# Kernel tuning notes

Measured on AMD Instinct MI355X. Metric: run time of the kernel, lower is better.

The kernel has to match this reference:

```python
import jax, jax.numpy as jnp
import numpy as np

EMBED_DIM = 2048
NUM_HEADS = 16
HEAD_DIM = EMBED_DIM // NUM_HEADS
BATCH, SEQ = 4, 4096


def setup_inputs() -> dict:
    key = jax.random.key(0)
    k1, k2, k3, k4 = jax.random.split(key, 4)
    scale = 1.0 / np.sqrt(EMBED_DIM)
    x = jax.random.normal(k1, (BATCH, SEQ, EMBED_DIM), dtype=jnp.float32)
    W_qkv = jax.random.normal(k2, (EMBED_DIM, 3 * EMBED_DIM), dtype=jnp.float32) * scale
    W_out = jax.random.normal(k3, (EMBED_DIM, EMBED_DIM), dtype=jnp.float32) * scale
    b_out = jax.random.normal(k4, (EMBED_DIM,), dtype=jnp.float32) * 0.01
    return {"x": x, "W_qkv": W_qkv, "W_out": W_out, "b_out": b_out}


def reference(x, W_qkv, W_out, b_out):
    b, s, _ = x.shape
    # qkv: (b, s, 3, h, d)
    qkv = (x @ W_qkv).reshape(b, s, 3, NUM_HEADS, HEAD_DIM)
    q, k, v = qkv[:, :, 0], qkv[:, :, 1], qkv[:, :, 2]
    # NOTE: faithful to source — scores mix HEADS per token: (b, s, h, h)
    scores = jnp.einsum('bshd,bsHd->bshH', q, k) / jnp.sqrt(jnp.float32(HEAD_DIM))
    w = jax.nn.softmax(scores, axis=-1)
    attn = jnp.einsum('bshH,bsHd->bshd', w, v).reshape(b, s, EMBED_DIM)
    return attn @ W_out + b_out
```

## Files before the change

### kernel.cpp

```cpp
#include <hip/hip_runtime.h>
#include <hip/hip_bf16.h>
#include <cstdint>


#define TOKENS 16384
#define EMB    2048
#define NQKV   6144

typedef __bf16 bf16x8_t __attribute__((ext_vector_type(8)));
typedef float  f32x4_t  __attribute__((ext_vector_type(4)));

#define GLOAD16(gsrc, ldst)                                                    \
  __builtin_amdgcn_global_load_lds(                                            \
      (const __attribute__((address_space(1))) void*)(uintptr_t)(gsrc),        \
      (__attribute__((address_space(3))) void*)(uint32_t)(uintptr_t)(ldst),    \
      16, 0, 0)

static __device__ __forceinline__ unsigned short f32_to_bf16_bits(float f) {
  union { float f; uint32_t u; } x; x.f = f;
  uint32_t u = x.u;
  u += 0x7fffu + ((u >> 16) & 1u);
  return (unsigned short)(u >> 16);
}

__global__ __launch_bounds__(256) void prep(
    const float4* __restrict__ x4, ushort4* __restrict__ xb4,
    const float* __restrict__ Wqkv, unsigned short* __restrict__ wqkvT,
    const float* __restrict__ Wout, unsigned short* __restrict__ woutT) {
  const int b = blockIdx.x;
  const int t = threadIdx.x;
  if (b < 2048) {
    const int n4 = 33554432 / 4;
    const int stride = 2048 * 256;
    for (int i = b * 256 + t; i < n4; i += stride) {
      float4 v = x4[i];
      ushort4 o;
      o.x = f32_to_bf16_bits(v.x);
      o.y = f32_to_bf16_bits(v.y);
      o.z = f32_to_bf16_bits(v.z);
      o.w = f32_to_bf16_bits(v.w);
      xb4[i] = o;
    }
    return;
  }
  __shared__ float tile[32][33];
  const float* in;
  unsigned short* out;
  int R, C, bxt, byt;
  if (b < 14336) {
    const int bb = b - 2048;
    in = Wqkv; out = wqkvT; R = 2048; C = 6144;
    bxt = bb % 192; byt = bb / 192;
  } else {
    const int bb = b - 14336;
    in = Wout; out = woutT; R = 2048; C = 2048;
    bxt = bb % 64; byt = bb / 64;
  }
  const int bx = bxt * 32;
  const int by = byt * 32;
  const int tx = t & 31;
  const int ty = t >> 5;
#pragma unroll
  for (int j = 0; j < 32; j += 8)
    tile[ty + j][tx] = in[(size_t)(by + ty + j) * C + bx + tx];
  __syncthreads();
#pragma unroll
  for (int j = 0; j < 32; j += 8)
    out[(size_t)(bx + ty + j) * R + by + tx] = f32_to_bf16_bits(tile[tx][ty + j]);
}

template <bool OUT_BF16>
__global__ __launch_bounds__(512, 1) void gemm_bt(
    const unsigned short* __restrict__ A,
    const unsigned short* __restrict__ BT,
    unsigned short* __restrict__ Cb,
    float* __restrict__ Cf,
    const float* __restrict__ bias,
    int M, int N) {
  constexpr int K = 2048;
  constexpr int BK = 64;
  constexpr int NKT = K / BK;
  __shared__ __align__(16) char lds[131072];

  const int nbx = N / 256;
  const int nwg = gridDim.x;
  const int bid = blockIdx.x;
  const int swzb = (bid & 7) * (nwg >> 3) + (bid >> 3);
  const int by = swzb / nbx;
  const int bx = swzb % nbx;

  const int t    = threadIdx.x;
  const int lane = t & 63;
  const int wid  = t >> 6;
  const int wr   = wid >> 2;
  const int wc   = wid & 3;
  const int lr   = lane & 15;
  const int g    = lane >> 4;

  const unsigned short* aSrc = A  + (size_t)by * 256 * K;
  const unsigned short* bSrc = BT + (size_t)bx * 256 * K;

  int aoff[2], boff[2];
#pragma unroll
  for (int i = 0; i < 2; ++i) {
    const int p   = (i * 512 + t) * 16;
    const int lo  = p ^ (((p >> 7) & 7) << 4);
    const int rih = lo >> 7;
    const int kbe = (lo & 127) >> 1;
    aoff[i] = (((rih >> 6) << 7) + (rih & 63)) * K + kbe;
    boff[i] = (((rih >> 5) << 6) + (rih & 31)) * K + kbe;
  }
  const int ldst = wid << 10;

  auto stageA = [&](int h, int k0, char* bufA) {
#pragma unroll
    for (int i = 0; i < 2; ++i)
      GLOAD16(aSrc + aoff[i] + h * (64 * K) + k0, bufA + h * 16384 + i * 8192 + ldst);
  };
  auto stageB = [&](int h, int k0, char* bufB) {
#pragma unroll
    for (int i = 0; i < 2; ++i)
      GLOAD16(bSrc + boff[i] + h * (32 * K) + k0, bufB + h * 16384 + i * 8192 + ldst);
  };

  const int sw   = (lr & 7) << 4;
  const int col0 = (g * 16) ^ sw;
  const int col1 = (64 + g * 16) ^ sw;
  const int aRow = (wr * 64 + lr) * 128;
  const int bRow = (wc * 32 + lr) * 128;

  f32x4_t acc[8][4] = {};
  bf16x8_t av[4][2];
  bf16x8_t bvA[2][2], bvB[2][2];
  bf16x8_t bv1[2][2];

#define LDA_INTO(dst, bufA_, q)                                                \
  {                                                                            \
    const char* _b = (bufA_) + (q) * 16384 + aRow;                             \
    _Pragma("unroll") for (int m2 = 0; m2 < 4; ++m2) {                         \
      dst[m2][0] = *(const bf16x8_t*)(_b + m2 * 2048 + col0);                  \
      dst[m2][1] = *(const bf16x8_t*)(_b + m2 * 2048 + col1);                  \
    }                                                                          \
  }
#define LDB_INTO(dst, bufB_, pair)                                             \
  {                                                                            \
    _Pragma("unroll") for (int e = 0; e < 2; ++e) {                            \
      const int nf = (pair) * 2 + e;                                           \
      const char* _b = (bufB_) + (nf >> 1) * 16384 + (nf & 1) * 2048 + bRow;   \
      dst[e][0] = *(const bf16x8_t*)(_b + col0);                               \
      dst[e][1] = *(const bf16x8_t*)(_b + col1);                               \
    }                                                                          \
  }
#define MFMAQ(AV, BV, Q, PAIR)                                                 \
  _Pragma("unroll") for (int m2 = 0; m2 < 4; ++m2)                             \
  _Pragma("unroll") for (int e = 0; e < 2; ++e)                                \
  _Pragma("unroll") for (int ks = 0; ks < 2; ++ks)                             \
    acc[(Q) * 4 + m2][(PAIR) * 2 + e] = __builtin_amdgcn_mfma_f32_16x16x32_bf16( \
        AV[m2][ks], BV[e][ks], acc[(Q) * 4 + m2][(PAIR) * 2 + e], 0, 0, 0);
#define MFMAQ_M(AV, BV, Q, PAIR, M0)                                           \
  _Pragma("unroll") for (int m2 = (M0); m2 < (M0) + 2; ++m2)                   \
  _Pragma("unroll") for (int e = 0; e < 2; ++e)                                \
  _Pragma("unroll") for (int ks = 0; ks < 2; ++ks)                             \
    acc[(Q) * 4 + m2][(PAIR) * 2 + e] = __builtin_amdgcn_mfma_f32_16x16x32_bf16( \
        AV[m2][ks], BV[e][ks], acc[(Q) * 4 + m2][(PAIR) * 2 + e], 0, 0, 0);
#define MFMAQ_E(AV, BV, Q, PAIR, E)                                            \
  _Pragma("unroll") for (int m2 = 0; m2 < 4; ++m2)                             \
  _Pragma("unroll") for (int ks = 0; ks < 2; ++ks)                             \
    acc[(Q) * 4 + m2][(PAIR) * 2 + (E)] = __builtin_amdgcn_mfma_f32_16x16x32_bf16( \
        AV[m2][ks], BV[(E)][ks], acc[(Q) * 4 + m2][(PAIR) * 2 + (E)], 0, 0, 0);

#define SBR __builtin_amdgcn_sched_barrier(0)
#define BARR __builtin_amdgcn_s_barrier()
#define LGKM(NN) asm volatile("s_waitcnt lgkmcnt(" #NN ")" ::: "memory"); SBR;
#define P1_ __builtin_amdgcn_s_setprio(1);
#define P0_ __builtin_amdgcn_s_setprio(0); SBR;

#define BODY(KT, BVC, BVN, S1, S2, VMN)                                        \
  {                                                                            \
    char* cA = lds + ((KT) & 1) * 65536;                                       \
    char* cB = cA + 32768;                                                     \
    char* nB = lds + (((KT) + 1) & 1) * 65536 + 32768;                         \
    const int k1 = ((KT) + 1) * BK, k2 = ((KT) + 2) * BK;                      \
                                 \
    LDA_INTO(av, cA, 0); SBR;                                                  \
    if (S1) { stageB(0, k1, nB); } SBR;                                        \
    BARR; LGKM(4); P1_;                                                        \
    MFMAQ_M(av, BVC, 0, 0, 0);                                                 \
    LGKM(0);                                                                   \
    MFMAQ_M(av, BVC, 0, 0, 2);                                                 \
    P0_; BARR;                                                                 \
                                                                   \
    LDB_INTO(bv1, cB, 1); SBR;                                                 \
    if (S2) { stageA(0, k2, cA); } SBR;                                        \
    BARR; LGKM(2); P1_;                                                        \
    MFMAQ_E(av, bv1, 0, 1, 0);                                                 \
    LGKM(0);                                                                   \
    MFMAQ_E(av, bv1, 0, 1, 1);                                                 \
    P0_; BARR;                                                                 \
                  \
    LDA_INTO(av, cA, 1); SBR;                                                  \
    if (S2) { stageB(1, k2, cB); } SBR;                                        \
    BARR; LGKM(4); P1_;                                                        \
    MFMAQ_M(av, bv1, 1, 1, 0);                                                 \
    LGKM(0);                                                                   \
    MFMAQ_M(av, bv1, 1, 1, 2);                                                 \
    P0_; BARR;                                                                 \
         \
    if (S2) { stageA(1, k2, cA); } SBR;                                        \
    asm volatile("s_waitcnt vmcnt(" #VMN ")" ::: "memory"); SBR;               \
    BARR;                                                                      \
    if (S1) { LDB_INTO(BVN, nB, 0); } SBR;                                     \
    P1_;                                                                       \
    MFMAQ(av, BVC, 1, 0);                                                      \
    P0_; BARR;                                                                 \
  }

  {
    char* b0A = lds;
    char* b0B = lds + 32768;
    char* b1A = lds + 65536;
    char* b1B = b1A + 32768;
    stageA(0, 0, b0A); stageA(1, 0, b0A);
    stageB(0, 0, b0B); stageB(1, 0, b0B);
    stageA(0, BK, b1A);
    stageB(1, BK, b1B);
    stageA(1, BK, b1A);
    asm volatile("s_waitcnt vmcnt(6)" ::: "memory");
    BARR;
    LDB_INTO(bvA, b0B, 0);
    SBR;
  }

  for (int kt = 0; kt < NKT - 2; kt += 2) {
    BODY(kt,     bvA, bvB, 1, 1, 6);
    BODY(kt + 1, bvB, bvA, 1, 1, 6);
  }
  BODY(NKT - 2, bvA, bvB, 1, 0, 0);
  BODY(NKT - 1, bvB, bvA, 0, 0, 0);

  const int rbase = by * 256 + wr * 128 + g * 4;
  const int cbase = bx * 256 + wc * 64 + lr;
#pragma unroll
  for (int m = 0; m < 8; ++m) {
#pragma unroll
    for (int nf = 0; nf < 4; ++nf) {
      const int col = cbase + nf * 16;
#pragma unroll
      for (int j = 0; j < 4; ++j) {
        const size_t off = (size_t)(rbase + (m >> 2) * 64 + (m & 3) * 16 + j) * N + col;
        if constexpr (OUT_BF16) {
          Cb[off] = f32_to_bf16_bits(acc[m][nf][j]);
        } else {
          Cf[off] = acc[m][nf][j] + bias[col];
        }
      }
    }
  }
#undef LDA_INTO
#undef LDB_INTO
#undef MFMAQ
#undef MFMAQ_M
#undef MFMAQ_E
#undef SBR
#undef BARR
#undef LGKM
#undef P1_
#undef P0_
#undef BODY
}

__global__ __launch_bounds__(256) void attn_heads(
    const unsigned short* __restrict__ qkv,
    unsigned short* __restrict__ attn) {
  __shared__ __align__(16) unsigned short sQKV[NQKV];
  __shared__ float sW[16][16];

  const int t = threadIdx.x;
  const size_t qbase = (size_t)blockIdx.x * NQKV;

  const uint4* gp = (const uint4*)(qkv + qbase);
  uint4* l = (uint4*)sQKV;
#pragma unroll
  for (int i = 0; i < 3; ++i) {
    const int idx = i * 256 + t;
    int dst = idx;
    if (idx >= 256 && idx < 512) {
      const int r = (idx - 256) >> 4;
      const int c = idx & 15;
      dst = 256 + r * 16 + (c ^ (r & 7));
    }
    l[dst] = gp[idx];
  }
  __syncthreads();

  const int h = t >> 4;
  const int H = t & 15;
  const bf16x8_t* q8 = (const bf16x8_t*)sQKV + h * 16;
  const bf16x8_t* k8 = (const bf16x8_t*)sQKV + 256;
  float s = 0.f;
#pragma unroll
  for (int d8 = 0; d8 < 16; ++d8) {
    bf16x8_t qv = q8[d8];
    bf16x8_t kv = k8[H * 16 + (d8 ^ (H & 7))];
#pragma unroll
    for (int j = 0; j < 8; ++j)
      s = fmaf((float)qv[j], (float)kv[j], s);
  }
  s *= 0.08838834764831843f;

  float mx = s;
#pragma unroll
  for (int o = 8; o; o >>= 1) mx = fmaxf(mx, __shfl_xor(mx, o));
  const float e = __expf(s - mx);
  float sum = e;
#pragma unroll
  for (int o = 8; o; o >>= 1) sum += __shfl_xor(sum, o);
  sW[h][H] = e / sum;
  __syncthreads();

  const int d0c = t & 15;
  const bf16x8_t* v8 = (const bf16x8_t*)sQKV + 512;
  float accv[8] = {};
#pragma unroll
  for (int j = 0; j < 16; ++j) {
    const float w = sW[h][j];
    const bf16x8_t vv = v8[j * 16 + d0c];
#pragma unroll
    for (int jj = 0; jj < 8; ++jj)
      accv[jj] = fmaf(w, (float)vv[jj], accv[jj]);
  }
  bf16x8_t o;
#pragma unroll
  for (int jj = 0; jj < 8; ++jj) o[jj] = (__bf16)accv[jj];
  *(bf16x8_t*)(attn + (size_t)blockIdx.x * EMB + h * 128 + d0c * 8) = o;
}

extern "C" void kernel_launch(void* const* d_in, const int* in_sizes, int n_in,
                              void* d_out, int out_size, void* d_ws, size_t ws_size,
                              hipStream_t stream) {
  const float* x    = (const float*)d_in[0];
  const float* Wqkv = (const float*)d_in[1];
  const float* Wout = (const float*)d_in[2];
  const float* bout = (const float*)d_in[3];
  float* out = (float*)d_out;

  unsigned short* xb    = (unsigned short*)d_ws;
  unsigned short* wqkvT = xb    + (size_t)33554432;
  unsigned short* woutT = wqkvT + (size_t)12582912;
  unsigned short* qkv   = woutT + (size_t)4194304;
  unsigned short* attn  = qkv   + (size_t)100663296;

  prep<<<18432, 256, 0, stream>>>((const float4*)x, (ushort4*)xb,
                                  Wqkv, wqkvT, Wout, woutT);
  gemm_bt<true><<<(16384 / 256) * (6144 / 256), 512, 0, stream>>>(
      xb, wqkvT, qkv, nullptr, nullptr, 16384, 6144);
  attn_heads<<<TOKENS, 256, 0, stream>>>(qkv, attn);
  gemm_bt<false><<<(16384 / 256) * (2048 / 256), 512, 0, stream>>>(
      attn, woutT, nullptr, out, bout, 16384, 2048);
}
```

Before: 609.9 us.

## Restructure GEMM main loop into ping-pong wave groups alternating LDS loads and MFMA

Rewrites the GEMM K-loop so the two wave rows act as ping-pong groups. One group reads its A/B fragments from LDS while the other runs its MFMA quarter, and the roles swap at each barrier. This replaces the earlier schedule, where every wave interleaved fragment loads and MFMAs using partial lgkmcnt waits and a B fragment carried across iterations. The global staging order and vmcnt depth change to match. The aim is to overlap LDS traffic and MFMA across waves. The cost is extra barriers and a one-phase skew that needs a trailing MFMA step after the loop.

```diff
diff --git a/kernel.cpp b/kernel.cpp
--- a/kernel.cpp
+++ b/kernel.cpp
@@ -96,6 +96,7 @@
   const int wc   = wid & 3;
   const int lr   = lane & 15;
   const int g    = lane >> 4;
+  const bool g0  = (wr == 0);
 
   const unsigned short* aSrc = A  + (size_t)by * 256 * K;
   const unsigned short* bSrc = BT + (size_t)bx * 256 * K;
@@ -131,8 +132,7 @@
 
   f32x4_t acc[8][4] = {};
   bf16x8_t av[4][2];
-  bf16x8_t bvA[2][2], bvB[2][2];
-  bf16x8_t bv1[2][2];
+  bf16x8_t bv0[2][2], bv1[2][2];
 
 #define LDA_INTO(dst, bufA_, q)                                                \
   {                                                                            \
@@ -157,86 +157,65 @@
   _Pragma("unroll") for (int ks = 0; ks < 2; ++ks)                             \
     acc[(Q) * 4 + m2][(PAIR) * 2 + e] = __builtin_amdgcn_mfma_f32_16x16x32_bf16( \
         AV[m2][ks], BV[e][ks], acc[(Q) * 4 + m2][(PAIR) * 2 + e], 0, 0, 0);
-#define MFMAQ_M(AV, BV, Q, PAIR, M0)                                           \
-  _Pragma("unroll") for (int m2 = (M0); m2 < (M0) + 2; ++m2)                   \
-  _Pragma("unroll") for (int e = 0; e < 2; ++e)                                \
-  _Pragma("unroll") for (int ks = 0; ks < 2; ++ks)                             \
-    acc[(Q) * 4 + m2][(PAIR) * 2 + e] = __builtin_amdgcn_mfma_f32_16x16x32_bf16( \
-        AV[m2][ks], BV[e][ks], acc[(Q) * 4 + m2][(PAIR) * 2 + e], 0, 0, 0);
-#define MFMAQ_E(AV, BV, Q, PAIR, E)                                            \
-  _Pragma("unroll") for (int m2 = 0; m2 < 4; ++m2)                             \
-  _Pragma("unroll") for (int ks = 0; ks < 2; ++ks)                             \
-    acc[(Q) * 4 + m2][(PAIR) * 2 + (E)] = __builtin_amdgcn_mfma_f32_16x16x32_bf16( \
-        AV[m2][ks], BV[(E)][ks], acc[(Q) * 4 + m2][(PAIR) * 2 + (E)], 0, 0, 0);
 
 #define SBR __builtin_amdgcn_sched_barrier(0)
 #define BARR __builtin_amdgcn_s_barrier()
-#define LGKM(NN) asm volatile("s_waitcnt lgkmcnt(" #NN ")" ::: "memory"); SBR;
+#define LGKM0 asm volatile("s_waitcnt lgkmcnt(0)" ::: "memory"); SBR;
 #define P1_ __builtin_amdgcn_s_setprio(1);
 #define P0_ __builtin_amdgcn_s_setprio(0); SBR;
 
-#define BODY(KT, BVC, BVN, S1, S2, VMN)                                        \
+#define MQ0 { LGKM0; P1_; MFMAQ(av, bv0, 0, 0); MFMAQ(av, bv1, 0, 1); P0_; }
+#define MQ1 { LGKM0; P1_; MFMAQ(av, bv0, 1, 0); MFMAQ(av, bv1, 1, 1); P0_; }
+
+#define BODY(KT, SA1, SB2, VMN, MP)                                            \
   {                                                                            \
     char* cA = lds + ((KT) & 1) * 65536;                                       \
     char* cB = cA + 32768;                                                     \
-    char* nB = lds + (((KT) + 1) & 1) * 65536 + 32768;                         \
+    char* nA = lds + (((KT) + 1) & 1) * 65536;                                 \
     const int k1 = ((KT) + 1) * BK, k2 = ((KT) + 2) * BK;                      \
-                                 \
-    LDA_INTO(av, cA, 0); SBR;                                                  \
-    if (S1) { stageB(0, k1, nB); } SBR;                                        \
-    BARR; LGKM(4); P1_;                                                        \
-    MFMAQ_M(av, BVC, 0, 0, 0);                                                 \
-    LGKM(0);                                                                   \
-    MFMAQ_M(av, BVC, 0, 0, 2);                                                 \
-    P0_; BARR;                                                                 \
-                                                                   \
-    LDB_INTO(bv1, cB, 1); SBR;                                                 \
-    if (S2) { stageA(0, k2, cA); } SBR;                                        \
-    BARR; LGKM(2); P1_;                                                        \
-    MFMAQ_E(av, bv1, 0, 1, 0);                                                 \
-    LGKM(0);                                                                   \
-    MFMAQ_E(av, bv1, 0, 1, 1);                                                 \
-    P0_; BARR;                                                                 \
-                  \
-    LDA_INTO(av, cA, 1); SBR;                                                  \
-    if (S2) { stageB(1, k2, cB); } SBR;                                        \
-    BARR; LGKM(4); P1_;                                                        \
-    MFMAQ_M(av, bv1, 1, 1, 0);                                                 \
-    LGKM(0);                                                                   \
-    MFMAQ_M(av, bv1, 1, 1, 2);                                                 \
-    P0_; BARR;                                                                 \
-         \
-    if (S2) { stageA(1, k2, cA); } SBR;                                        \
+               \
+    if (g0) { LDA_INTO(av, cA, 0); LDB_INTO(bv0, cB, 0); LDB_INTO(bv1, cB, 1); } \
+    SBR;                                                                       \
+    if (SA1) { stageA(0, k1, nA); } SBR;                                       \
+    if (!g0 && (MP)) MQ1;                                                      \
+    SBR; BARR;                                                                 \
+                        \
+    if (!g0) { LDA_INTO(av, cA, 0); LDB_INTO(bv0, cB, 0); LDB_INTO(bv1, cB, 1); } \
+    SBR;                                                                       \
+    if (SA1) { stageA(1, k1, nA); } SBR;                                       \
+    if (g0) MQ0;                                                               \
+    SBR; BARR;                                                                 \
+                                         \
+    if (g0) { LDA_INTO(av, cA, 1); } SBR;                                      \
+    if (!g0) MQ0;                                                              \
+    SBR; BARR;                                                                 \
+                   \
+    if (!g0) { LDA_INTO(av, cA, 1); } SBR;                                     \
+    if (SB2) { stageB(0, k2, cB); stageB(1, k2, cB); } SBR;                    \
     asm volatile("s_waitcnt vmcnt(" #VMN ")" ::: "memory"); SBR;               \
-    BARR;                                                                      \
-    if (S1) { LDB_INTO(BVN, nB, 0); } SBR;                                     \
-    P1_;                                                                       \
-    MFMAQ(av, BVC, 1, 0);                                                      \
-    P0_; BARR;                                                                 \
+    if (g0) MQ1;                                                               \
+    SBR; BARR;                                                                 \
   }
 
   {
     char* b0A = lds;
     char* b0B = lds + 32768;
-    char* b1A = lds + 65536;
-    char* b1B = b1A + 32768;
-    stageA(0, 0, b0A); stageA(1, 0, b0A);
+    char* b1B = lds + 65536 + 32768;
     stageB(0, 0, b0B); stageB(1, 0, b0B);
-    stageA(0, BK, b1A);
-    stageB(1, BK, b1B);
-    stageA(1, BK, b1A);
-    asm volatile("s_waitcnt vmcnt(6)" ::: "memory");
+    stageA(0, 0, b0A);
+    stageA(1, 0, b0A);
+    stageB(0, BK, b1B); stageB(1, BK, b1B);
+    asm volatile("s_waitcnt vmcnt(4)" ::: "memory");
     BARR;
-    LDB_INTO(bvA, b0B, 0);
-    SBR;
-  }
-
-  for (int kt = 0; kt < NKT - 2; kt += 2) {
-    BODY(kt,     bvA, bvB, 1, 1, 6);
-    BODY(kt + 1, bvB, bvA, 1, 1, 6);
-  }
-  BODY(NKT - 2, bvA, bvB, 1, 0, 0);
-  BODY(NKT - 1, bvB, bvA, 0, 0, 0);
+  }
+
+  BODY(0, 1, 1, 4, 0);
+  for (int kt = 1; kt < NKT - 2; ++kt) {
+    BODY(kt, 1, 1, 4, 1);
+  }
+  BODY(NKT - 2, 1, 0, 0, 1);
+  BODY(NKT - 1, 0, 0, 0, 1);
+  if (!g0) MQ1;
 
   const int rbase = by * 256 + wr * 128 + g * 4;
   const int cbase = bx * 256 + wc * 64 + lr;
@@ -259,13 +238,13 @@
 #undef LDA_INTO
 #undef LDB_INTO
 #undef MFMAQ
-#undef MFMAQ_M
-#undef MFMAQ_E
 #undef SBR
 #undef BARR
-#undef LGKM
+#undef LGKM0
 #undef P1_
 #undef P0_
+#undef MQ0
+#undef MQ1
 #undef BODY
 }
 
```

Measured after the change: 598.2 us. About the same (-1.9%).
